# Kernel optimization log

Hardware: AMD Instinct MI355X
Metric: run time of the kernel (lower is better)

## Reference

```python
import jax, jax.numpy as jnp
import numpy as np

D_EMBED = 512
N_HEAD = 8
N_LAYER = 12
B, S = 4, 1024


def setup_inputs() -> dict:
    key = jax.random.key(0)
    ks = jax.random.split(key, 8)
    std = 0.02
    x = jax.random.normal(ks[0], (B, S, D_EMBED), dtype=jnp.float32)
    e = jax.random.normal(ks[1], (B, S, D_EMBED), dtype=jnp.float32)
    p = jax.random.normal(ks[2], (S, D_EMBED), dtype=jnp.float32)
    W_q = std * jax.random.normal(ks[3], (N_HEAD, D_EMBED, D_EMBED), dtype=jnp.float32)
    W_k = std * jax.random.normal(ks[4], (N_HEAD, D_EMBED, D_EMBED), dtype=jnp.float32)
    W_v = std * jax.random.normal(ks[5], (N_HEAD, D_EMBED, D_EMBED), dtype=jnp.float32)
    # torch Linear weight: (out_features, in_features) = (E, H*E)
    W_o = (std / np.sqrt(2 * N_LAYER)) * jax.random.normal(ks[6], (D_EMBED, N_HEAD * D_EMBED), dtype=jnp.float32)
    gamma = std * jax.random.normal(ks[7], (1, N_HEAD, 1, 1), dtype=jnp.float32)
    return {"x": x, "e": e, "p": p, "W_q": W_q, "W_k": W_k, "W_v": W_v, "W_o": W_o, "gamma": gamma}


def reference(x, e, p, W_q, W_k, W_v, W_o, gamma):
    # use_ppe_attn=False path: Q,K,V all from x. Per-head full-dim projections.
    Q = jnp.einsum('bse,hef->bhsf', x, W_q)  # (B,H,S,E)
    K = jnp.einsum('bse,hef->bhsf', x, W_k)
    V = jnp.einsum('bse,hef->bhsf', x, W_v)
    # rbf kernel: exp(-gamma * ||q - k||_2^2), squared distance via expansion
    q2 = jnp.sum(Q * Q, axis=-1, keepdims=True)          # (B,H,S,1)
    k2 = jnp.sum(K * K, axis=-1, keepdims=True)          # (B,H,S,1)
    qk = jnp.einsum('bhse,bhte->bhst', Q, K)             # (B,H,S,S)
    d2 = jnp.maximum(q2 + jnp.swapaxes(k2, -2, -1) - 2.0 * qk, 0.0)
    attn = jnp.exp(-gamma * d2)                          # (B,H,S,S)
    out = jnp.einsum('bhst,bhte->bhse', attn, V)         # (B,H,S,E)
    out = jnp.transpose(out, (0, 2, 1, 3)).reshape(x.shape[0], x.shape[1], -1)  # (B,S,H*E)
    return out @ W_o.T                                   # (B,S,E)
```

## Files before the change

kernel.cpp:

```cpp
#include <hip/hip_runtime.h>
#include <cstdint>
#include <cstring>

typedef unsigned short ushort_t;
typedef __attribute__((ext_vector_type(8))) short short8;
typedef __attribute__((ext_vector_type(4))) float f32x4;
typedef __attribute__((ext_vector_type(4))) unsigned short us4;

constexpr int Hh = 8;
constexpr int Ss = 1024;
constexpr int Ee = 512;

__device__ __forceinline__ ushort_t f2bf(float f) {
    uint32_t u; __builtin_memcpy(&u, &f, 4);
    u += 0x7fffu + ((u >> 16) & 1u);
    return (ushort_t)(u >> 16);
}
__device__ __forceinline__ float bf2f(ushort_t h) {
    uint32_t u = ((uint32_t)h) << 16; float f; __builtin_memcpy(&f, &u, 4); return f;
}

__device__ __forceinline__ void gload_lds16(const ushort_t* g, void* lds) {
    __builtin_amdgcn_global_load_lds(
        (const __attribute__((address_space(1))) void*)g,
        (__attribute__((address_space(3))) void*)lds, 16, 0, 0);
}


__global__ void cvt_f32_bf16(const float4* __restrict__ in, us4* __restrict__ out, int n4) {
    int i = blockIdx.x * blockDim.x + threadIdx.x;
    if (i < n4) {
        float4 v = in[i];
        us4 o = { f2bf(v.x), f2bf(v.y), f2bf(v.z), f2bf(v.w) };
        out[i] = o;
    }
}

__global__ void wtrans(const float* __restrict__ W, ushort_t* __restrict__ Wt) {
    __shared__ float tile[32][33];
    int h = blockIdx.z;
    int e0 = blockIdx.y * 32, f0 = blockIdx.x * 32;
    int tx = threadIdx.x, ty = threadIdx.y;
    #pragma unroll
    for (int i = 0; i < 4; i++) {
        int e = e0 + ty + i * 8;
        tile[ty + i * 8][tx] = W[((size_t)h * 512 + e) * 512 + f0 + tx];
    }
    __syncthreads();
    #pragma unroll
    for (int i = 0; i < 4; i++) {
        int f = f0 + ty + i * 8;
        Wt[((size_t)h * 512 + f) * 512 + e0 + tx] = f2bf(tile[tx][ty + i * 8]);
    }
}

__global__ void sumsq(const ushort_t* __restrict__ X, float* __restrict__ out) {
    int row = blockIdx.x * 4 + (threadIdx.x >> 6);
    int ln = threadIdx.x & 63;
    short8 v = *(const short8*)(X + (size_t)row * 512 + ln * 8);
    float s = 0.f;
    #pragma unroll
    for (int j = 0; j < 8; j++) {
        float f = bf2f((ushort_t)v[j]);
        s += f * f;
    }
    #pragma unroll
    for (int off = 32; off > 0; off >>= 1) s += __shfl_xor(s, off);
    if (ln == 0) out[row] = s;
}

__global__ void reduce8(const f32x4* __restrict__ p, f32x4* __restrict__ out, int n4) {
    int i = blockIdx.x * blockDim.x + threadIdx.x;
    if (i < n4) {
        f32x4 a = p[i];
        #pragma unroll
        for (int j = 1; j < 8; j++) a += p[i + (size_t)j * n4];
        out[i] = a;
    }
}

template<int EPI>
__global__ __launch_bounds__(512, 1)
void gemm256(const ushort_t* __restrict__ A, int lda,
             const ushort_t* __restrict__ Bm, int ldb,
             void* __restrict__ Cout, int K,
             const float* __restrict__ q2, const float* __restrict__ k2,
             const float* __restrict__ gamma, int bIdx)
{
    __shared__ __align__(16) ushort_t SMEM[65536];

    const int t  = threadIdx.x;
    const int wv = t >> 6, ln = t & 63;
    const int wm = wv >> 2, wn = wv & 3;

    const int gx = gridDim.x, gy = gridDim.y;
    const int nwg = gx * gy * gridDim.z;
    const int L = blockIdx.x + gx * (blockIdx.y + gy * blockIdx.z);
    const int wid = (L & 7) * (nwg >> 3) + (L >> 3);
    const int bx = wid % gx;
    const int tmp = wid / gx;
    const int by = tmp % gy;
    const int z  = tmp / gy;

    const int m0 = by * 256, n0 = bx * 256;

    int bh = z;
    if constexpr (EPI == 2 || EPI == 3) bh = (bIdx < 0) ? z : (bIdx * Hh + z);

    const ushort_t* Ab = A;
    const ushort_t* Bb = Bm;
    if constexpr (EPI == 0 || EPI == 1) { Bb = Bm + (size_t)z * Ee * Ee; }
    if constexpr (EPI == 2) {
        Ab = A  + (size_t)bh * Ss * Ee;
        Bb = Bm + (size_t)bh * Ss * Ee;
    }
    if constexpr (EPI == 3) {
        Ab = A  + (size_t)z * Ss * Ss;
        Bb = Bm + (size_t)bh * Ee * Ss;
    }
    if constexpr (EPI == 4) {
        Ab = A  + (size_t)z * 512;
        Bb = Bm + (size_t)z * 512;
    }

    f32x4 acc[8][4];
    #pragma unroll
    for (int i = 0; i < 8; i++)
        #pragma unroll
        for (int j = 0; j < 4; j++) acc[i][j] = (f32x4){0.f, 0.f, 0.f, 0.f};

    const int srow = ln >> 3;
    const int schk = ((ln & 7) ^ srow) * 8;
    auto STAGE = [&](int ti, int buf) {
        const int k0 = ti << 6;
        #pragma unroll
        for (int c = 0; c < 8; ++c) {
            const int q = c * 8 + wv;
            const int idx = q & 31;
            const int rb = idx * 8 + srow;
            if (q < 32) {
                gload_lds16(Ab + (size_t)(m0 + rb) * lda + k0 + schk,
                            &SMEM[buf * 16384 + idx * 512]);
            } else {
                gload_lds16(Bb + (size_t)(n0 + rb) * ldb + k0 + schk,
                            &SMEM[32768 + buf * 16384 + idx * 512]);
            }
        }
    };

    const int T = K >> 6;
    STAGE(0, 0);
    __syncthreads();

    const int lrow = ln & 15, lkg = ln >> 4;
    const int swz = lrow & 7;

    int cur = 0;
    for (int ti = 0; ti < T; ++ti) {
        if (ti + 1 < T) STAGE(ti + 1, cur ^ 1);

        short8 bf[4][2];
        #pragma unroll
        for (int fc = 0; fc < 4; fc++)
            #pragma unroll
            for (int kg = 0; kg < 2; kg++)
                bf[fc][kg] = *(const short8*)(&SMEM[32768 + cur * 16384 +
                                                    (wn * 64 + fc * 16 + lrow) * 64 +
                                                    (((kg * 4 + lkg) ^ swz) << 3)]);
        #pragma unroll
        for (int hp = 0; hp < 2; hp++) {
            short8 af[4][2];
            #pragma unroll
            for (int f2 = 0; f2 < 4; f2++)
                #pragma unroll
                for (int kg = 0; kg < 2; kg++)
                    af[f2][kg] = *(const short8*)(&SMEM[cur * 16384 +
                                                        (wm * 128 + (hp * 4 + f2) * 16 + lrow) * 64 +
                                                        (((kg * 4 + lkg) ^ swz) << 3)]);
            __builtin_amdgcn_s_setprio(1);
            #pragma unroll
            for (int f2 = 0; f2 < 4; f2++)
                #pragma unroll
                for (int fc = 0; fc < 4; fc++)
                    #pragma unroll
                    for (int kg = 0; kg < 2; kg++)
                        acc[hp * 4 + f2][fc] = __builtin_amdgcn_mfma_f32_16x16x32_bf16(
                            af[f2][kg], bf[fc][kg], acc[hp * 4 + f2][fc], 0, 0, 0);
            __builtin_amdgcn_s_setprio(0);
        }

        __syncthreads();
        cur ^= 1;
    }

    const int crow = (ln >> 4) * 4, ccol = ln & 15;

    if constexpr (EPI == 1) {
        ushort_t* O = (ushort_t*)Cout;
        #pragma unroll
        for (int fr = 0; fr < 8; fr++) {
            #pragma unroll
            for (int fc = 0; fc < 4; fc++) {
                int gm0 = m0 + wm * 128 + fr * 16 + crow;
                int gn  = n0 + wn * 64 + fc * 16 + ccol;
                int b = gm0 >> 10, s = gm0 & 1023;
                us4 pk = { f2bf(acc[fr][fc][0]), f2bf(acc[fr][fc][1]),
                           f2bf(acc[fr][fc][2]), f2bf(acc[fr][fc][3]) };
                *(us4*)(O + ((size_t)(b * Hh + z) * Ee + gn) * Ss + s) = pk;
            }
        }
    } else if constexpr (EPI == 4) {
        float* O = (float*)Cout + (size_t)z * 4096 * 512;
        float* fscr = (float*)SMEM + wv * 2176;
        for (int pass = 0; pass < 4; ++pass) {
            #pragma unroll
            for (int fr2 = 0; fr2 < 2; fr2++) {
                int fr = pass * 2 + fr2;
                #pragma unroll
                for (int fc = 0; fc < 4; fc++)
                    #pragma unroll
                    for (int i = 0; i < 4; i++)
                        fscr[(fr2 * 16 + crow + i) * 68 + fc * 16 + ccol] = acc[fr][fc][i];
            }
            #pragma unroll
            for (int rr = 0; rr < 8; ++rr) {
                int r = rr * 4 + (ln >> 4);
                int c = (ln & 15) * 4;
                f32x4 v = *(const f32x4*)&fscr[r * 68 + c];
                int gm = m0 + wm * 128 + pass * 32 + r;
                int gn = n0 + wn * 64 + c;
                *(f32x4*)&O[(size_t)gm * 512 + gn] = v;
            }
        }
    } else {
        ushort_t* scr = SMEM + wv * 4608;
        float g = 0.f; const float* q2b = nullptr; const float* k2b = nullptr;
        float k2v[4];
        if constexpr (EPI == 2) {
            g = gamma[z & 7];
            q2b = q2 + (size_t)bh * Ss;
            k2b = k2 + (size_t)bh * Ss;
            #pragma unroll
            for (int fc = 0; fc < 4; fc++) k2v[fc] = k2b[n0 + wn * 64 + fc * 16 + ccol];
        }
        for (int pass = 0; pass < 2; ++pass) {
            float q2p[4][4];
            if constexpr (EPI == 2) {
                #pragma unroll
                for (int fr2 = 0; fr2 < 4; fr2++)
                    #pragma unroll
                    for (int i = 0; i < 4; i++)
                        q2p[fr2][i] = q2b[m0 + wm * 128 + pass * 64 + fr2 * 16 + crow + i];
            }
            #pragma unroll
            for (int fr2 = 0; fr2 < 4; fr2++) {
                int fr = pass * 4 + fr2;
                #pragma unroll
                for (int fc = 0; fc < 4; fc++) {
                    #pragma unroll
                    for (int i = 0; i < 4; i++) {
                        float v = acc[fr][fc][i];
                        if constexpr (EPI == 2) {
                            float d2 = fmaxf(q2p[fr2][i] + k2v[fc] - 2.0f * v, 0.0f);
                            v = __expf(-g * d2);
                        }
                        scr[(fr2 * 16 + crow + i) * 72 + fc * 16 + ccol] = f2bf(v);
                    }
                }
            }
            #pragma unroll
            for (int rr = 0; rr < 8; ++rr) {
                int r = rr * 8 + (ln >> 3);
                int c = (ln & 7) * 8;
                short8 v = *(const short8*)&scr[r * 72 + c];
                int gm = m0 + wm * 128 + pass * 64 + r;
                int gn = n0 + wn * 64 + c;
                ushort_t* O = (ushort_t*)Cout;
                size_t addr;
                if constexpr (EPI == 0) {
                    int b = gm >> 10, s = gm & 1023;
                    addr = ((size_t)(b * Hh + z) * Ss + s) * Ee + gn;
                } else if constexpr (EPI == 2) {
                    addr = ((size_t)z * Ss + gm) * Ss + gn;
                } else {
                    int bo = (bIdx < 0) ? (z >> 3) : bIdx;
                    int hh = (bIdx < 0) ? (z & 7) : z;
                    addr = ((size_t)(bo * Ss + gm)) * (Hh * Ee) + (size_t)hh * Ee + gn;
                }
                *(short8*)&O[addr] = v;
            }
        }
    }
}


extern "C" void kernel_launch(void* const* d_in, const int* in_sizes, int n_in,
                              void* d_out, int out_size, void* d_ws, size_t ws_size,
                              hipStream_t stream)
{
    const float* x     = (const float*)d_in[0];
    const float* Wq    = (const float*)d_in[3];
    const float* Wk    = (const float*)d_in[4];
    const float* Wv    = (const float*)d_in[5];
    const float* Wo    = (const float*)d_in[6];
    const float* gamma = (const float*)d_in[7];

    char* ws = (char*)d_ws;
    size_t off = 0;
    auto alloc = [&](size_t bytes) -> void* {
        void* p = ws + off;
        off += (bytes + 255) & ~(size_t)255;
        return p;
    };
    ushort_t* xb    = (ushort_t*)alloc(4096ull * 512 * 2);
    ushort_t* WqT   = (ushort_t*)alloc(8ull * 512 * 512 * 2);
    ushort_t* WkT   = (ushort_t*)alloc(8ull * 512 * 512 * 2);
    ushort_t* WvT   = (ushort_t*)alloc(8ull * 512 * 512 * 2);
    ushort_t* WoB   = (ushort_t*)alloc(512ull * 4096 * 2);
    ushort_t* Qb    = (ushort_t*)alloc(4ull * 8 * 1024 * 512 * 2);
    ushort_t* Kb    = (ushort_t*)alloc(4ull * 8 * 1024 * 512 * 2);
    ushort_t* Vt    = (ushort_t*)alloc(4ull * 8 * 512 * 1024 * 2);
    float*    q2    = (float*)alloc(32768ull * 4);
    float*    k2    = (float*)alloc(32768ull * 4);

    size_t off_common = off;
    size_t need_merged = off_common + 64ull * 1024 * 1024;
    bool merged = (ws_size >= need_merged);

    ushort_t* attn;
    ushort_t* Ob;
    float* fpart;
    if (merged) {
        attn = (ushort_t*)alloc(32ull * 1024 * 1024 * 2);
        Ob   = Qb;
        fpart = (float*)attn;
    } else {
        attn = (ushort_t*)alloc(8ull * 1024 * 1024 * 2);
        Ob   = (ushort_t*)alloc(4096ull * 4096 * 2);
        fpart = (float*)Qb;
    }
    (void)in_sizes; (void)n_in; (void)out_size;

    cvt_f32_bf16<<<2048, 256, 0, stream>>>((const float4*)x,  (us4*)xb,  524288);
    cvt_f32_bf16<<<2048, 256, 0, stream>>>((const float4*)Wo, (us4*)WoB, 524288);

    dim3 tb(32, 8);
    wtrans<<<dim3(16, 16, 8), tb, 0, stream>>>(Wq, WqT);
    wtrans<<<dim3(16, 16, 8), tb, 0, stream>>>(Wk, WkT);
    wtrans<<<dim3(16, 16, 8), tb, 0, stream>>>(Wv, WvT);

    gemm256<0><<<dim3(2, 16, 8), 512, 0, stream>>>(xb, 512, WqT, 512, Qb, 512, nullptr, nullptr, nullptr, 0);
    gemm256<0><<<dim3(2, 16, 8), 512, 0, stream>>>(xb, 512, WkT, 512, Kb, 512, nullptr, nullptr, nullptr, 0);
    gemm256<1><<<dim3(2, 16, 8), 512, 0, stream>>>(xb, 512, WvT, 512, Vt, 512, nullptr, nullptr, nullptr, 0);

    sumsq<<<16384, 256, 0, stream>>>(Qb, q2);

    if (merged) {
        gemm256<2><<<dim3(4, 4, 32), 512, 0, stream>>>(Qb, 512, Kb, 512, attn, 512, q2, k2, gamma, -1);
        gemm256<3><<<dim3(2, 4, 32), 512, 0, stream>>>(attn, 1024, Vt, 1024, Ob, 1024, nullptr, nullptr, nullptr, -1);
    } else {
        for (int b = 0; b < 4; b++) {
            gemm256<2><<<dim3(4, 4, 8), 512, 0, stream>>>(Qb, 512, Kb, 512, attn, 512, q2, k2, gamma, b);
            gemm256<3><<<dim3(2, 4, 8), 512, 0, stream>>>(attn, 1024, Vt, 1024, Ob, 1024, nullptr, nullptr, nullptr, b);
        }
    }

    gemm256<4><<<dim3(2, 16, 8), 512, 0, stream>>>(Ob, 4096, WoB, 4096, fpart, 512, nullptr, nullptr, nullptr, 0);
    reduce8<<<2048, 256, 0, stream>>>((const f32x4*)fpart, (f32x4*)d_out, 524288);
}
```

Before: 221.5 us.

## Interleave fine-grained LDS staging with MFMA phases using explicit vmcnt waits

Restructures the GEMM main loop into eight phases per pair of K-tiles. Each phase issues one quarter-tile of global-to-LDS loads for upcoming tiles and runs a slice of MFMAs, gated by explicit s_waitcnt vmcnt counts and raw s_barrier calls in place of a whole-tile __syncthreads. The aim is to spread memory traffic across the compute and avoid the full drain at each tile boundary. In exchange it adds a barrier per phase, depends on the vmcnt bookkeeping being correct, and assumes an even tile count.

```diff
diff --git a/kernel.cpp b/kernel.cpp
--- a/kernel.cpp
+++ b/kernel.cpp
@@ -131,67 +131,100 @@
 
     const int srow = ln >> 3;
     const int schk = ((ln & 7) ^ srow) * 8;
-    auto STAGE = [&](int ti, int buf) {
-        const int k0 = ti << 6;
+    auto STAGE_UNIT = [&](int tile, int kind) {
+        const int k0 = tile << 6;
+        const int base = (kind < 2 ? 0 : 32768) + (tile & 1) * 16384;
+        const int half = kind & 1;
         #pragma unroll
-        for (int c = 0; c < 8; ++c) {
-            const int q = c * 8 + wv;
-            const int idx = q & 31;
+        for (int c = 0; c < 2; ++c) {
+            const int idx = half * 16 + wv * 2 + c;
             const int rb = idx * 8 + srow;
-            if (q < 32) {
-                gload_lds16(Ab + (size_t)(m0 + rb) * lda + k0 + schk,
-                            &SMEM[buf * 16384 + idx * 512]);
-            } else {
-                gload_lds16(Bb + (size_t)(n0 + rb) * ldb + k0 + schk,
-                            &SMEM[32768 + buf * 16384 + idx * 512]);
-            }
+            const ushort_t* src = (kind < 2)
+                ? Ab + (size_t)(m0 + rb) * lda + k0 + schk
+                : Bb + (size_t)(n0 + rb) * ldb + k0 + schk;
+            gload_lds16(src, &SMEM[base + idx * 512]);
         }
     };
 
     const int T = K >> 6;
-    STAGE(0, 0);
-    __syncthreads();
+
+    #pragma unroll
+    for (int kk = 0; kk < 4; ++kk) STAGE_UNIT(0, kk);
+    #pragma unroll
+    for (int kk = 0; kk < 4; ++kk) STAGE_UNIT(1, kk);
+    asm volatile("s_waitcnt vmcnt(8)" ::: "memory");
+    __builtin_amdgcn_sched_barrier(0);
+    __builtin_amdgcn_s_barrier();
+    __builtin_amdgcn_sched_barrier(0);
 
     const int lrow = ln & 15, lkg = ln >> 4;
     const int swz = lrow & 7;
 
-    int cur = 0;
-    for (int ti = 0; ti < T; ++ti) {
-        if (ti + 1 < T) STAGE(ti + 1, cur ^ 1);
-
-        short8 bf[4][2];
+    for (int u = 0; u < (T >> 1); ++u) {
+        short8 bfr[4][2];
         #pragma unroll
-        for (int fc = 0; fc < 4; fc++)
-            #pragma unroll
-            for (int kg = 0; kg < 2; kg++)
-                bf[fc][kg] = *(const short8*)(&SMEM[32768 + cur * 16384 +
-                                                    (wn * 64 + fc * 16 + lrow) * 64 +
-                                                    (((kg * 4 + lkg) ^ swz) << 3)]);
-        #pragma unroll
-        for (int hp = 0; hp < 2; hp++) {
-            short8 af[4][2];
-            #pragma unroll
-            for (int f2 = 0; f2 < 4; f2++)
-                #pragma unroll
-                for (int kg = 0; kg < 2; kg++)
-                    af[f2][kg] = *(const short8*)(&SMEM[cur * 16384 +
-                                                        (wm * 128 + (hp * 4 + f2) * 16 + lrow) * 64 +
-                                                        (((kg * 4 + lkg) ^ swz) << 3)]);
-            __builtin_amdgcn_s_setprio(1);
-            #pragma unroll
-            for (int f2 = 0; f2 < 4; f2++)
+        for (int p = 0; p < 8; ++p) {
+            const int d = p >> 2, q = p & 3;
+
+            if (p == 0 && u > 0) {
+                if (2 * u + 1 < T) asm volatile("s_waitcnt vmcnt(4)" ::: "memory");
+                else               asm volatile("s_waitcnt vmcnt(0)" ::: "memory");
+            }
+            if (p == 4) {
+                if (2 * u + 2 < T) asm volatile("s_waitcnt vmcnt(4)" ::: "memory");
+                else               asm volatile("s_waitcnt vmcnt(0)" ::: "memory");
+            }
+            __builtin_amdgcn_sched_barrier(0);
+            __builtin_amdgcn_s_barrier();
+            __builtin_amdgcn_sched_barrier(0);
+
+            if (q == 0) {
                 #pragma unroll
                 for (int fc = 0; fc < 4; fc++)
                     #pragma unroll
                     for (int kg = 0; kg < 2; kg++)
-                        acc[hp * 4 + f2][fc] = __builtin_amdgcn_mfma_f32_16x16x32_bf16(
-                            af[f2][kg], bf[fc][kg], acc[hp * 4 + f2][fc], 0, 0, 0);
+                        bfr[fc][kg] = *(const short8*)(&SMEM[32768 + d * 16384 +
+                                          (wn * 64 + fc * 16 + lrow) * 64 +
+                                          (((kg * 4 + lkg) ^ swz) << 3)]);
+            }
+            short8 af[2][2];
+            #pragma unroll
+            for (int j = 0; j < 2; j++)
+                #pragma unroll
+                for (int kg = 0; kg < 2; kg++)
+                    af[j][kg] = *(const short8*)(&SMEM[d * 16384 +
+                                     (wm * 128 + (q * 2 + j) * 16 + lrow) * 64 +
+                                     (((kg * 4 + lkg) ^ swz) << 3)]);
+
+            {
+                int stile, skind;
+                if      (p == 0) { stile = 2 * u + 1; skind = 0; }
+                else if (p == 1) { stile = 2 * u + 1; skind = 1; }
+                else if (p == 2) { stile = 2 * u + 2; skind = 2; }
+                else if (p == 3) { stile = 2 * u + 2; skind = 3; }
+                else if (p == 4) { stile = 2 * u + 2; skind = 0; }
+                else if (p == 5) { stile = 2 * u + 2; skind = 1; }
+                else if (p == 6) { stile = 2 * u + 3; skind = 2; }
+                else             { stile = 2 * u + 3; skind = 3; }
+                if (stile < T && !(u == 0 && stile == 1))
+                    STAGE_UNIT(stile, skind);
+            }
+
+            __builtin_amdgcn_s_setprio(1);
+            #pragma unroll
+            for (int j = 0; j < 2; j++)
+                #pragma unroll
+                for (int fc = 0; fc < 4; fc++)
+                    #pragma unroll
+                    for (int kg = 0; kg < 2; kg++)
+                        acc[q * 2 + j][fc] = __builtin_amdgcn_mfma_f32_16x16x32_bf16(
+                            af[j][kg], bfr[fc][kg], acc[q * 2 + j][fc], 0, 0, 0);
             __builtin_amdgcn_s_setprio(0);
         }
-
-        __syncthreads();
-        cur ^= 1;
-    }
+    }
+    __builtin_amdgcn_sched_barrier(0);
+    __builtin_amdgcn_s_barrier();
+    __builtin_amdgcn_sched_barrier(0);
 
     const int crow = (ln >> 4) * 4, ccol = ln & 15;
 
@@ -289,6 +322,7 @@
                 }
                 *(short8*)&O[addr] = v;
             }
+            __builtin_amdgcn_s_barrier();
         }
     }
 }
```

Measured after the change: 220.6 us. No clear change (-0.4%).
